# Kernel optimization log

Measured on AMD Instinct MI355X. Metric: run time of the kernel, lower is better.

## Reference

```python
import jax, jax.numpy as jnp
import numpy as np

EMBED_DIM = 768
NUM_HEADS = 12
HEAD_DIM = EMBED_DIM // NUM_HEADS
MAX_REL = 50
B, L = 4, 1024


def setup_inputs() -> dict:
    key = jax.random.key(0)
    ks = jax.random.split(key, 8)
    query = jax.random.normal(ks[0], (B, L, EMBED_DIM), dtype=jnp.float32)
    k_in = jax.random.normal(ks[1], (B, L, EMBED_DIM), dtype=jnp.float32)
    v_in = jax.random.normal(ks[2], (B, L, EMBED_DIM), dtype=jnp.float32)
    # monotone float timestamps per batch (arange fill)
    patch_indices = jnp.arange(B * L, dtype=jnp.float32).reshape(B, L)
    std = 1.0 / np.sqrt(EMBED_DIM)
    in_proj_w = jax.random.normal(ks[3], (3 * EMBED_DIM, EMBED_DIM), dtype=jnp.float32) * std
    in_proj_b = jnp.zeros((3 * EMBED_DIM,), dtype=jnp.float32)
    out_proj_w = jax.random.normal(ks[4], (EMBED_DIM, EMBED_DIM), dtype=jnp.float32) * std
    out_proj_b = jnp.zeros((EMBED_DIM,), dtype=jnp.float32)
    rel_bias = jax.random.truncated_normal(ks[5], -2.0, 2.0, (NUM_HEADS, 2 * MAX_REL + 1), dtype=jnp.float32) * 0.1
    return {"query": query, "key": k_in, "value": v_in, "patch_indices": patch_indices,
            "in_proj_w": in_proj_w, "in_proj_b": in_proj_b,
            "out_proj_w": out_proj_w, "out_proj_b": out_proj_b, "rel_bias": rel_bias}


def _attention(query, patch_indices, in_proj_w, in_proj_b, out_proj_w, out_proj_b, rel_bias):
    Bq, Lq, D = query.shape
    H, hd, M = NUM_HEADS, HEAD_DIM, MAX_REL
    qkv = query @ in_proj_w.T + in_proj_b            # [B,L,3D]
    q, k, v = jnp.split(qkv, 3, axis=-1)
    q = q.reshape(Bq, Lq, H, hd).transpose(0, 2, 1, 3) * (hd ** -0.5)
    k = k.reshape(Bq, Lq, H, hd).transpose(0, 2, 1, 3)
    v = v.reshape(Bq, Lq, H, hd).transpose(0, 2, 1, 3)
    scores = jnp.einsum('bhld,bhmd->bhlm', q, k)     # [B,H,L,L]
    # sequence-position relative bias
    idxs = jnp.arange(Lq)
    rel_pos = jnp.clip(idxs[None, :] - idxs[:, None], -M, M) + M   # [L,L]
    scores = scores + rel_bias[:, rel_pos][None]                   # [1,H,L,L]
    # data-dependent relative-time bias
    deltas = patch_indices[:, 1:] - patch_indices[:, :-1]          # [B,L-1]
    dt = jnp.nanmedian(deltas, axis=1)
    dt = jnp.where(jnp.isfinite(dt) & (dt > 0), dt, 1.0)[:, None, None]
    rel_time = patch_indices[:, :, None] - patch_indices[:, None, :]  # [B,L,L]
    invalid = jnp.isnan(rel_time) | (rel_time < -M) | (rel_time > M)
    rel_time = jnp.where(invalid, 0.0, rel_time)
    rel_idx = (jnp.clip(jnp.round(rel_time / dt), -M, M) + M).astype(jnp.int32)  # [B,L,L]
    bias = jnp.take(rel_bias, rel_idx, axis=1)       # [H,B,L,L]
    scores = scores + jnp.moveaxis(bias, 0, 1)       # [B,H,L,L]
    probs = jax.nn.softmax(scores, axis=-1)
    out = jnp.einsum('bhlm,bhmd->bhld', probs, v)
    out = out.transpose(0, 2, 1, 3).reshape(Bq, Lq, D)
    return out @ out_proj_w.T + out_proj_b


def reference(query, key, value, patch_indices, in_proj_w, in_proj_b, out_proj_w, out_proj_b, rel_bias):
    # NOTE: the original module ignores key/value and builds qkv from query.
    return _attention(query, patch_indices, in_proj_w, in_proj_b, out_proj_w, out_proj_b, rel_bias)
```

## Files before the change

### kernel.cpp

```cpp
#include <hip/hip_runtime.h>
#include <hip/hip_bf16.h>

#define BB 4
#define LL 1024
#define DD 768
#define HH 12
#define HD 64
#define MREL 50
#define NBIAS 101
#define GK 768
#define STR 72
#define BXS 68

#define NEG_INF (-__builtin_inff())

#define QB_F   ((size_t)0)
#define KB_F   ((size_t)1572864)
#define VTB_F  ((size_t)3145728)
#define XBF_F  ((size_t)4718592)
#define WIBF_F ((size_t)6291456)
#define WOBF_F ((size_t)7176192)
#define BIDX_F ((size_t)7471104)
#define DT_F   ((size_t)9568256)

#define NQ4  (BB*LL*DD)
#define NWI4 (3*DD*DD)

typedef __attribute__((ext_vector_type(8)))  short bf16x8;
typedef __attribute__((ext_vector_type(4)))  float f32x4;
typedef __attribute__((ext_vector_type(16))) float f32x16;
typedef __attribute__((ext_vector_type(4)))  unsigned int u32x4;

__device__ __forceinline__ unsigned short f2bf(float f) {
    unsigned u = __float_as_uint(f);
    u += 0x7fffu + ((u >> 16) & 1u);
    return (unsigned short)(u >> 16);
}

__device__ __forceinline__ void gload_lds16(const void* g, void* l) {
    __builtin_amdgcn_global_load_lds(
        (const __attribute__((address_space(1))) void*)g,
        (__attribute__((address_space(3))) void*)l, 16, 0, 0);
}

__global__ __launch_bounds__(256) void prep_kernel(
    const float* __restrict__ patch, float* __restrict__ dt,
    const float* __restrict__ q, const float* __restrict__ wi, const float* __restrict__ wo,
    unsigned short* __restrict__ qd_, unsigned short* __restrict__ wid,
    unsigned short* __restrict__ wod) {
    int tid = threadIdx.x;
    if (blockIdx.x >= 4) {
        int i = ((blockIdx.x - 4) * 256 + tid) * 4;
        const float* src; unsigned short* dst; int off;
        if (i < NQ4)              { src = q;  dst = qd_; off = i; }
        else if (i < NQ4 + NWI4)  { src = wi; dst = wid; off = i - NQ4; }
        else                      { src = wo; dst = wod; off = i - NQ4 - NWI4; }
        float4 v = *(const float4*)&src[off];
        ushort4 o;
        o.x = f2bf(v.x); o.y = f2bf(v.y); o.z = f2bf(v.z); o.w = f2bf(v.w);
        *(ushort4*)&dst[off] = o;
        return;
    }
    __shared__ __align__(16) float del[1024];
    __shared__ __align__(16) unsigned long long key64[1024];
    __shared__ int nvalid;
    __shared__ float acc;
    int b = blockIdx.x;
    if (tid == 0) { nvalid = 0; acc = 0.f; }
    __syncthreads();
    int cnt = 0;
#pragma unroll
    for (int r = 0; r < 4; ++r) {
        int i = tid + r * 256;
        float v = __builtin_nanf("");
        if (i < LL - 1) {
            v = patch[b * LL + i + 1] - patch[b * LL + i];
            if (v == v) ++cnt;
        }
        del[i] = v;
        unsigned bits = (v == v) ? __float_as_uint(v) : 0x7FC00000u;
        unsigned ordk = (bits & 0x80000000u) ? ~bits : (bits | 0x80000000u);
        key64[i] = ((unsigned long long)ordk << 10) | (unsigned)i;
    }
    atomicAdd(&nvalid, cnt);
    __syncthreads();
    int i0 = tid, i1 = tid + 256, i2 = tid + 512, i3 = tid + 768;
    float v0 = del[i0], v1 = del[i1], v2 = del[i2], v3 = del[i3];
    unsigned long long k0 = key64[i0], k1 = key64[i1], k2 = key64[i2], k3 = key64[i3];
    int c0 = 0, c1 = 0, c2 = 0, c3 = 0;
#define CMPK(kx) { unsigned long long _k = (kx); \
    c0 += (_k < k0) ? 1 : 0; c1 += (_k < k1) ? 1 : 0; \
    c2 += (_k < k2) ? 1 : 0; c3 += (_k < k3) ? 1 : 0; }
    for (int j = 0; j < 1024; j += 8) {
        ulonglong2 a = *(const ulonglong2*)&key64[j];
        ulonglong2 bq = *(const ulonglong2*)&key64[j + 2];
        ulonglong2 cq = *(const ulonglong2*)&key64[j + 4];
        ulonglong2 dq = *(const ulonglong2*)&key64[j + 6];
        CMPK(a.x); CMPK(a.y); CMPK(bq.x); CMPK(bq.y);
        CMPK(cq.x); CMPK(cq.y); CMPK(dq.x); CMPK(dq.y);
    }
#undef CMPK
    int n = nvalid;
#define FIN(vr, cr) if (vr == vr) { \
    if (n & 1) { if (cr == n / 2) atomicAdd(&acc, vr); } \
    else { if (cr == n / 2 - 1 || cr == n / 2) atomicAdd(&acc, 0.5f * vr); } }
    FIN(v0, c0); FIN(v1, c1); FIN(v2, c2); FIN(v3, c3);
#undef FIN
    __syncthreads();
    if (tid == 0) {
        float m = acc;
        float res = (n > 0 && m == m && fabsf(m) != __builtin_inff() && m > 0.f) ? m : 1.0f;
        dt[b] = res;
    }
}

__global__ __launch_bounds__(256) void bidx_kernel(const float* __restrict__ patch,
                                                   const float* __restrict__ dtb,
                                                   unsigned short* __restrict__ bidx) {
    int flat = (blockIdx.x * 256 + threadIdx.x) * 8;
    int b = flat >> 20;
    int rem = flat & 1048575;
    int i = rem >> 10;
    int j0 = rem & 1023;
    float pi = patch[b * LL + i];
    float inv_dt = 1.0f / dtb[b];
    float4 pa = *(const float4*)&patch[b * LL + j0];
    float4 pb4 = *(const float4*)&patch[b * LL + j0 + 4];
    unsigned out[4];
#define MK(pj, jofs, dst, shift) { \
    int d = (j0 + jofs) - i; d = d < -MREL ? -MREL : (d > MREL ? MREL : d); \
    float rt = pi - (pj); \
    if (!(rt == rt) || rt < -(float)MREL || rt > (float)MREL) rt = 0.f; \
    float fr = fminf(fmaxf(rintf(rt * inv_dt), -(float)MREL), (float)MREL); \
    unsigned u = (unsigned)(d + MREL) | (((unsigned)((int)fr + MREL)) << 8); \
    dst |= (u << shift); }
    unsigned t;
    t = 0; MK(pa.x, 0, t, 0); MK(pa.y, 1, t, 16); out[0] = t;
    t = 0; MK(pa.z, 2, t, 0); MK(pa.w, 3, t, 16); out[1] = t;
    t = 0; MK(pb4.x, 4, t, 0); MK(pb4.y, 5, t, 16); out[2] = t;
    t = 0; MK(pb4.z, 6, t, 0); MK(pb4.w, 7, t, 16); out[3] = t;
#undef MK
    *(uint4*)&bidx[flat] = *(uint4*)&out[0];
}

#define GEMM_CORE(TN_, RB_, NT_)                                               \
    __shared__ unsigned short As[64 * 64];                                     \
    __shared__ unsigned short Bs[TN_ * 64];                                    \
    int tid = threadIdx.x;                                                     \
    int m0 = blockIdx.x << 6, n0 = blockIdx.y * TN_;                           \
    int lane = tid & 63, w = tid >> 6;                                         \
    int wn = w * (TN_ / 4);                                                    \
    int srow = tid >> 3, scol = (tid & 7) << 3;                                \
    const unsigned short* Ag = Ab + (size_t)(m0 + srow) * GK + scol;           \
    const unsigned short* Bg = Wb + (size_t)(n0 + srow) * GK + scol;           \
    f32x4 acc[4][NT_];                                                         \
    _Pragma("unroll") for (int i = 0; i < 4; ++i)                              \
        _Pragma("unroll") for (int j = 0; j < NT_; ++j)                        \
            acc[i][j] = (f32x4){0.f, 0.f, 0.f, 0.f};                           \
    int qd_ = lane >> 4;                                                       \
    int rA = lane & 15, rB = wn + (lane & 15);                                 \
    for (int kc = 0; kc < GK; kc += 64) {                                      \
        __syncthreads();                                                       \
        _Pragma("unroll") for (int r = 0; r < 2; ++r)                          \
            gload_lds16(Ag + (size_t)(r * 32) * GK + kc, As + tid * 8 + r * 2048); \
        _Pragma("unroll") for (int r = 0; r < RB_; ++r)                        \
            gload_lds16(Bg + (size_t)(r * 32) * GK + kc, Bs + tid * 8 + r * 2048); \
        __syncthreads();                                                       \
        _Pragma("unroll") for (int ks = 0; ks < 2; ++ks) {                     \
            bf16x8 af[4], bfr[NT_];                                            \
            _Pragma("unroll") for (int t = 0; t < 4; ++t)                      \
                af[t] = *(const bf16x8*)&As[(rA + t * 16) * 64 + ks * 32 + qd_ * 8]; \
            _Pragma("unroll") for (int t = 0; t < NT_; ++t)                    \
                bfr[t] = *(const bf16x8*)&Bs[(rB + t * 16) * 64 + ks * 32 + qd_ * 8]; \
            _Pragma("unroll") for (int i = 0; i < 4; ++i)                      \
                _Pragma("unroll") for (int j = 0; j < NT_; ++j)                \
                    acc[i][j] = __builtin_amdgcn_mfma_f32_16x16x32_bf16(       \
                        af[i], bfr[j], acc[i][j], 0, 0, 0);                    \
        }                                                                      \
    }                                                                          \
    int colL = lane & 15, rq = lane >> 4;

__global__ __launch_bounds__(256) void qkv_gemm(
    const unsigned short* __restrict__ Ab, const unsigned short* __restrict__ Wb,
    const float* __restrict__ bias,
    unsigned short* __restrict__ qb, unsigned short* __restrict__ kb,
    unsigned short* __restrict__ vtb) {
    GEMM_CORE(128, 4, 2);
    int sec = n0 / DD;
    float scale = (sec == 0) ? 0.18033688011112042f : 1.0f;
#pragma unroll
    for (int j = 0; j < 2; ++j) {
        int n = n0 + wn + j * 16 + colL;
        int d768 = n - sec * DD;
        int hh = d768 >> 6, dd = d768 & 63;
        float bn = bias[n];
#pragma unroll
        for (int i = 0; i < 4; ++i) {
            int rowb = m0 + i * 16 + rq * 4;
#pragma unroll
            for (int r = 0; r < 4; ++r) {
                int m = rowb + r;
                int bidx = m >> 10, l = m & 1023;
                unsigned short val = f2bf((acc[i][j][r] + bn) * scale);
                if (sec == 0)
                    qb[(((size_t)bidx * HH + hh) * LL + l) * HD + dd] = val;
                else if (sec == 1)
                    kb[(((size_t)bidx * HH + hh) * LL + l) * HD + dd] = val;
                else
                    vtb[(((size_t)bidx * HH + hh) * HD + dd) * LL + l] = val;
            }
        }
    }
}

__global__ __launch_bounds__(256) void out_gemm(
    const unsigned short* __restrict__ Ab, const unsigned short* __restrict__ Wb,
    const float* __restrict__ bias, float* __restrict__ C) {
    GEMM_CORE(64, 2, 1);
    {
        int n = n0 + wn + colL;
        float bn = bias[n];
#pragma unroll
        for (int i = 0; i < 4; ++i) {
            int rowb = m0 + i * 16 + rq * 4;
#pragma unroll
            for (int r = 0; r < 4; ++r)
                C[(size_t)(rowb + r) * DD + n] = acc[i][0][r] + bn;
        }
    }
}

__global__ __launch_bounds__(256) void attn_kernel(
    const unsigned short* __restrict__ QB, const unsigned short* __restrict__ KB,
    const unsigned short* __restrict__ VTB, const unsigned short* __restrict__ BIDX,
    const float* __restrict__ relb, unsigned short* __restrict__ aout) {
    __shared__ __align__(16) unsigned short smem[2 * 64 * STR + 64 * BXS];
    __shared__ float sb[NBIAS];
    __shared__ float psum_s[128];
    __shared__ float linv_s[64];
    unsigned short* Ks  = smem;
    unsigned short* Vt  = smem + 64 * STR;
    unsigned short* Bxs = smem + 2 * 64 * STR;
    float* fcomb = (float*)smem;

    int tid = threadIdx.x;
    int w = tid >> 6, lane = tid & 63, li = lane & 31, qd = lane >> 5;
    int jt = w & 1, it = w >> 1;
    int bh = blockIdx.x, b = bh / HH, h = bh - b * HH;
    int q0 = blockIdx.y << 6;
    if (tid < NBIAS) sb[tid] = relb[h * NBIAS + tid] * 1.44269504088896340736f;
    int i_loc = it * 32 + li;
    int i_abs = q0 + i_loc;
    bf16x8 kq[4];
    const unsigned short* qrow = QB + ((size_t)bh * LL + i_abs) * HD + qd * 8;
#pragma unroll
    for (int ks = 0; ks < 4; ++ks) kq[ks] = *(const bf16x8*)(qrow + ks * 16);
    float l_run = 0.f;
    f32x16 O0, O1;
#pragma unroll
    for (int r = 0; r < 16; ++r) { O0[r] = 0.f; O1[r] = 0.f; }
    int srow = tid >> 3, sc = (tid & 7) << 3;
    const unsigned short* kgb = KB + (size_t)bh * LL * HD;
    const unsigned short* vgb = VTB + (size_t)bh * HD * LL;
    const unsigned short* bxg = BIDX + ((size_t)b << 20) + (size_t)q0 * 1024;
    bf16x8 kvr[2], vvr[2], bxr[2];
#pragma unroll
    for (int rep = 0; rep < 2; ++rep) {
        int r = srow + rep * 32;
        kvr[rep] = *(const bf16x8*)(kgb + (size_t)r * HD + sc);
        vvr[rep] = *(const bf16x8*)(vgb + (size_t)r * LL + sc);
        bxr[rep] = *(const bf16x8*)(bxg + (size_t)r * 1024 + sc);
    }
    __syncthreads();
    float sb0 = sb[0], sb100 = sb[100];
    for (int kt = 0; kt < 16; ++kt) {
        __syncthreads();
#pragma unroll
        for (int rep = 0; rep < 2; ++rep) {
            int r = srow + rep * 32;
            *(bf16x8*)&Ks[r * STR + sc] = kvr[rep];
            *(bf16x8*)&Vt[r * STR + sc] = vvr[rep];
            *(bf16x8*)&Bxs[r * BXS + sc] = bxr[rep];
        }
        if (kt + 1 < 16) {
#pragma unroll
            for (int rep = 0; rep < 2; ++rep) {
                int r = srow + rep * 32;
                kvr[rep] = *(const bf16x8*)(kgb + (size_t)((kt + 1) * 64 + r) * HD + sc);
                vvr[rep] = *(const bf16x8*)(vgb + (size_t)r * LL + (kt + 1) * 64 + sc);
                bxr[rep] = *(const bf16x8*)(bxg + (size_t)r * 1024 + (kt + 1) * 64 + sc);
            }
        }
        __syncthreads();
        f32x16 st;
#pragma unroll
        for (int r = 0; r < 16; ++r) st[r] = 0.f;
#pragma unroll
        for (int ks = 0; ks < 4; ++ks) {
            bf16x8 ak = *(const bf16x8*)&Ks[(jt * 32 + li) * STR + ks * 16 + qd * 8];
            st = __builtin_amdgcn_mfma_f32_32x32x16_bf16(ak, kq[ks], st, 0, 0, 0);
        }
        int delta = (kt << 6) + (jt << 5) - q0 - (it << 5);
        if (delta >= 81 || delta <= -81) {
            float db = (delta >= 81) ? sb100 : sb0;
#pragma unroll
            for (int g4 = 0; g4 < 4; ++g4) {
                ushort4 bi = *(const ushort4*)&Bxs[i_loc * BXS + jt * 32 + g4 * 8 + qd * 4];
#pragma unroll
                for (int q = 0; q < 4; ++q) {
                    int r = g4 * 4 + q;
                    unsigned u = (q == 0) ? bi.x : (q == 1) ? bi.y : (q == 2) ? bi.z : bi.w;
                    st[r] = st[r] + db + sb[u >> 8];
                }
            }
        } else {
#pragma unroll
            for (int g4 = 0; g4 < 4; ++g4) {
                ushort4 bi = *(const ushort4*)&Bxs[i_loc * BXS + jt * 32 + g4 * 8 + qd * 4];
#pragma unroll
                for (int q = 0; q < 4; ++q) {
                    int r = g4 * 4 + q;
                    unsigned u = (q == 0) ? bi.x : (q == 1) ? bi.y : (q == 2) ? bi.z : bi.w;
                    st[r] = st[r] + sb[u & 0xffu] + sb[u >> 8];
                }
            }
        }
        float rs = 0.f;
        unsigned W[8];
#pragma unroll
        for (int pr = 0; pr < 8; ++pr) {
            float p0 = __builtin_amdgcn_exp2f(st[2 * pr]);
            float p1 = __builtin_amdgcn_exp2f(st[2 * pr + 1]);
            rs += p0 + p1;
            unsigned wpk;
            asm("v_cvt_pk_bf16_f32 %0, %1, %2" : "=v"(wpk) : "v"(p0), "v"(p1));
            W[pr] = wpk;
        }
        rs += __shfl_xor(rs, 32);
        l_run += rs;
        auto s02 = __builtin_amdgcn_permlane32_swap(W[0], W[2], false, false);
        auto s13 = __builtin_amdgcn_permlane32_swap(W[1], W[3], false, false);
        auto s46 = __builtin_amdgcn_permlane32_swap(W[4], W[6], false, false);
        auto s57 = __builtin_amdgcn_permlane32_swap(W[5], W[7], false, false);
        u32x4 a0w = {(unsigned)s02[0], (unsigned)s13[0], (unsigned)s02[1], (unsigned)s13[1]};
        u32x4 a1w = {(unsigned)s46[0], (unsigned)s57[0], (unsigned)s46[1], (unsigned)s57[1]};
        bf16x8 ap0 = __builtin_bit_cast(bf16x8, a0w);
        bf16x8 ap1 = __builtin_bit_cast(bf16x8, a1w);
        {
            bf16x8 bv;
            bv = *(const bf16x8*)&Vt[(li) * STR + jt * 32 + qd * 8];
            O0 = __builtin_amdgcn_mfma_f32_32x32x16_bf16(ap0, bv, O0, 0, 0, 0);
            bv = *(const bf16x8*)&Vt[(li) * STR + jt * 32 + 16 + qd * 8];
            O0 = __builtin_amdgcn_mfma_f32_32x32x16_bf16(ap1, bv, O0, 0, 0, 0);
            bv = *(const bf16x8*)&Vt[(32 + li) * STR + jt * 32 + qd * 8];
            O1 = __builtin_amdgcn_mfma_f32_32x32x16_bf16(ap0, bv, O1, 0, 0, 0);
            bv = *(const bf16x8*)&Vt[(32 + li) * STR + jt * 32 + 16 + qd * 8];
            O1 = __builtin_amdgcn_mfma_f32_32x32x16_bf16(ap1, bv, O1, 0, 0, 0);
        }
    }
    if (qd == 0) psum_s[jt * 64 + i_loc] = l_run;
    __syncthreads();
    if (jt == 0 && qd == 0)
        linv_s[i_loc] = 1.0f / (psum_s[i_loc] + psum_s[64 + i_loc]);
    if (jt == 1) {
        int ibase = it * 32;
#pragma unroll
        for (int r = 0; r < 16; ++r) {
            int irow = (r & 3) + ((r >> 2) << 3) + (qd << 2);
            fcomb[(ibase + irow) * 64 + li] = O0[r];
            fcomb[(ibase + irow) * 64 + 32 + li] = O1[r];
        }
    }
    __syncthreads();
    if (jt == 0) {
        int ibase = it * 32;
#pragma unroll
        for (int r = 0; r < 16; ++r) {
            int irow = (r & 3) + ((r >> 2) << 3) + (qd << 2);
            float inv = linv_s[ibase + irow];
            float v0 = (O0[r] + fcomb[(ibase + irow) * 64 + li]) * inv;
            float v1 = (O1[r] + fcomb[(ibase + irow) * 64 + 32 + li]) * inv;
            size_t rowoff = (size_t)(b * LL + q0 + ibase + irow) * DD + h * HD;
            aout[rowoff + li] = f2bf(v0);
            aout[rowoff + 32 + li] = f2bf(v1);
        }
    }
}

extern "C" void kernel_launch(void* const* d_in, const int* in_sizes, int n_in,
                              void* d_out, int out_size, void* d_ws, size_t ws_size,
                              hipStream_t stream) {
    const float* query    = (const float*)d_in[0];
    const float* patch    = (const float*)d_in[3];
    const float* in_w     = (const float*)d_in[4];
    const float* in_b     = (const float*)d_in[5];
    const float* out_w    = (const float*)d_in[6];
    const float* out_b    = (const float*)d_in[7];
    const float* rel_bias = (const float*)d_in[8];
    float* ws  = (float*)d_ws;
    float* out = (float*)d_out;

    unsigned short* qb   = (unsigned short*)(ws + QB_F);
    unsigned short* kb   = (unsigned short*)(ws + KB_F);
    unsigned short* vtb  = (unsigned short*)(ws + VTB_F);
    unsigned short* xbf  = (unsigned short*)(ws + XBF_F);
    unsigned short* wibf = (unsigned short*)(ws + WIBF_F);
    unsigned short* wobf = (unsigned short*)(ws + WOBF_F);
    unsigned short* bidx = (unsigned short*)(ws + BIDX_F);

    prep_kernel<<<5380, 256, 0, stream>>>(patch, ws + DT_F, query, in_w, out_w,
                                          xbf, wibf, wobf);
    bidx_kernel<<<2048, 256, 0, stream>>>(patch, ws + DT_F, bidx);
    qkv_gemm<<<dim3(64, 18), 256, 0, stream>>>(xbf, wibf, in_b, qb, kb, vtb);
    attn_kernel<<<dim3(BB * HH, LL / 64), 256, 0, stream>>>(
        qb, kb, vtb, bidx, rel_bias, xbf);
    out_gemm<<<dim3(64, 12), 256, 0, stream>>>(xbf, wobf, out_b, out);
}
```

Baseline: 203.8 us.

## Transpose V tile through LDS for coalesced stores; raise wave priority around MFMAs

The QKV GEMM epilogue for the V section now stages the bias-added bf16 tile in shared memory, transposed, then writes 16-byte vectors of contiguous sequence positions into the transposed V buffer. Previously each lane wrote scattered 2-byte values with a stride of LL. This targets the uncoalesced write traffic of the V transpose, at the cost of an extra LDS round trip and two barriers. Separately, the attention kernel wraps its QK and PV MFMA blocks in s_setprio to favour matrix issue across waves.

```diff
diff --git a/kernel.cpp b/kernel.cpp
--- a/kernel.cpp
+++ b/kernel.cpp
@@ -144,8 +144,9 @@
 }
 
 #define GEMM_CORE(TN_, RB_, NT_)                                               \
-    __shared__ unsigned short As[64 * 64];                                     \
-    __shared__ unsigned short Bs[TN_ * 64];                                    \
+    __shared__ __align__(16) unsigned short smem_g[64 * 64 + TN_ * 64];        \
+    unsigned short* As = smem_g;                                               \
+    unsigned short* Bs = smem_g + 64 * 64;                                     \
     int tid = threadIdx.x;                                                     \
     int m0 = blockIdx.x << 6, n0 = blockIdx.y * TN_;                           \
     int lane = tid & 63, w = tid >> 6;                                         \
@@ -187,6 +188,34 @@
     unsigned short* __restrict__ vtb) {
     GEMM_CORE(128, 4, 2);
     int sec = n0 / DD;
+    if (sec == 2) {
+        __syncthreads();
+        unsigned short* Ts = smem_g;
+#pragma unroll
+        for (int j = 0; j < 2; ++j) {
+            int nl = wn + j * 16 + colL;
+            float bn = bias[n0 + nl];
+#pragma unroll
+            for (int i = 0; i < 4; ++i) {
+                ushort4 o;
+                o.x = f2bf(acc[i][j][0] + bn);
+                o.y = f2bf(acc[i][j][1] + bn);
+                o.z = f2bf(acc[i][j][2] + bn);
+                o.w = f2bf(acc[i][j][3] + bn);
+                *(ushort4*)&Ts[nl * 72 + i * 16 + rq * 4] = o;
+            }
+        }
+        __syncthreads();
+        int row = tid >> 1, half = tid & 1;
+        int d768 = n0 + row - 2 * DD;
+        int hh = d768 >> 6, dd = d768 & 63;
+        unsigned short* dst = vtb + (((size_t)(m0 >> 10) * HH + hh) * HD + dd) * LL
+                              + (m0 & 1023) + half * 32;
+#pragma unroll
+        for (int k = 0; k < 4; ++k)
+            *(uint4*)&dst[k * 8] = *(const uint4*)&Ts[row * 72 + half * 32 + k * 8];
+        return;
+    }
     float scale = (sec == 0) ? 0.18033688011112042f : 1.0f;
 #pragma unroll
     for (int j = 0; j < 2; ++j) {
@@ -204,10 +233,8 @@
                 unsigned short val = f2bf((acc[i][j][r] + bn) * scale);
                 if (sec == 0)
                     qb[(((size_t)bidx * HH + hh) * LL + l) * HD + dd] = val;
-                else if (sec == 1)
+                else
                     kb[(((size_t)bidx * HH + hh) * LL + l) * HD + dd] = val;
-                else
-                    vtb[(((size_t)bidx * HH + hh) * HD + dd) * LL + l] = val;
             }
         }
     }
@@ -295,11 +322,13 @@
         f32x16 st;
 #pragma unroll
         for (int r = 0; r < 16; ++r) st[r] = 0.f;
+        __builtin_amdgcn_s_setprio(1);
 #pragma unroll
         for (int ks = 0; ks < 4; ++ks) {
             bf16x8 ak = *(const bf16x8*)&Ks[(jt * 32 + li) * STR + ks * 16 + qd * 8];
             st = __builtin_amdgcn_mfma_f32_32x32x16_bf16(ak, kq[ks], st, 0, 0, 0);
         }
+        __builtin_amdgcn_s_setprio(0);
         int delta = (kt << 6) + (jt << 5) - q0 - (it << 5);
         if (delta >= 81 || delta <= -81) {
             float db = (delta >= 81) ? sb100 : sb0;
@@ -347,6 +376,7 @@
         bf16x8 ap0 = __builtin_bit_cast(bf16x8, a0w);
         bf16x8 ap1 = __builtin_bit_cast(bf16x8, a1w);
         {
+            __builtin_amdgcn_s_setprio(1);
             bf16x8 bv;
             bv = *(const bf16x8*)&Vt[(li) * STR + jt * 32 + qd * 8];
             O0 = __builtin_amdgcn_mfma_f32_32x32x16_bf16(ap0, bv, O0, 0, 0, 0);
@@ -356,6 +386,7 @@
             O1 = __builtin_amdgcn_mfma_f32_32x32x16_bf16(ap0, bv, O1, 0, 0, 0);
             bv = *(const bf16x8*)&Vt[(32 + li) * STR + jt * 32 + 16 + qd * 8];
             O1 = __builtin_amdgcn_mfma_f32_32x32x16_bf16(ap1, bv, O1, 0, 0, 0);
+            __builtin_amdgcn_s_setprio(0);
         }
     }
     if (qd == 0) psum_s[jt * 64 + i_loc] = l_run;
```

Result: slower. 209.9 us (+3.0%).
